# Kernel tuning notes

Measured on AMD Instinct MI355X. Metric: run time of the kernel, lower is better.

The kernel has to match this reference:

```python
import jax, jax.numpy as jnp
import numpy as np

NU, NI, E = 100000, 20000, 250000
H, HEADS, D, L = 128, 2, 64, 2


def setup_inputs() -> dict:
    key = jax.random.key(0)
    ks = jax.random.split(key, 12)
    s = 0.05  # glorot-ish init scale
    return {
        "x_user": jax.random.normal(ks[0], (NU, 64), jnp.float32),
        "x_item": jax.random.normal(ks[1], (NI, 128), jnp.float32),
        "Wp_user": jax.random.normal(ks[2], (64, H), jnp.float32) * s,
        "bp_user": jnp.zeros((H,), jnp.float32),
        "Wp_item": jax.random.normal(ks[3], (128, H), jnp.float32) * s,
        "bp_item": jnp.zeros((H,), jnp.float32),
        # stacked per [layer, relation] params; rel 0 = user->item, rel 1 = item->user
        "Wl": jax.random.normal(ks[4], (L, 2, H, H), jnp.float32) * s,  # source linear
        "bl": jnp.zeros((L, 2, H), jnp.float32),
        "Wr": jax.random.normal(ks[5], (L, 2, H, H), jnp.float32) * s,  # target linear
        "br": jnp.zeros((L, 2, H), jnp.float32),
        "att": jax.random.normal(ks[6], (L, 2, HEADS, D), jnp.float32) * s,
        "bias": jnp.zeros((L, 2, H), jnp.float32),
        "edge_src": jax.random.randint(ks[7], (E,), 0, NU, jnp.int32),  # user index per edge
        "edge_dst": jax.random.randint(ks[8], (E,), 0, NI, jnp.int32),  # item index per edge
    }


def _gatv2(x_src, x_dst, src, dst, wl, bl_, wr, br_, a, b_, n_dst):
    """One bipartite GATv2Conv (heads=HEADS, out=D, concat=True, eval mode)."""
    xl = (x_src @ wl + bl_).reshape(-1, HEADS, D)  # [Ns, h, d]
    xr = (x_dst @ wr + br_).reshape(-1, HEADS, D)  # [Nd, h, d]
    e = jax.nn.leaky_relu(xl[src] + xr[dst], 0.2)  # [E, h, d]
    logits = jnp.einsum('ehd,hd->eh', e, a)        # [E, h]
    # segment softmax over destination nodes (numerically stable)
    amax = jax.lax.stop_gradient(jax.ops.segment_max(logits, dst, num_segments=n_dst))
    p = jnp.exp(logits - amax[dst])
    denom = jax.ops.segment_sum(p, dst, num_segments=n_dst)
    alpha = p / (denom[dst] + 1e-16)               # PyG softmax epsilon
    msg = xl[src] * alpha[:, :, None]              # [E, h, d]
    out = jax.ops.segment_sum(msg, dst, num_segments=n_dst)  # [Nd, h, d]
    return out.reshape(n_dst, HEADS * D) + b_


def reference(x_user, x_item, Wp_user, bp_user, Wp_item, bp_item,
              Wl, bl, Wr, br, att, bias, edge_src, edge_dst):
    zu = x_user @ Wp_user + bp_user  # [NU, H]
    zi = x_item @ Wp_item + bp_item  # [NI, H]
    for l in range(L):
        zi_new = _gatv2(zu, zi, edge_src, edge_dst,
                        Wl[l, 0], bl[l, 0], Wr[l, 0], br[l, 0], att[l, 0], bias[l, 0], NI)
        zu_new = _gatv2(zi, zu, edge_dst, edge_src,
                        Wl[l, 1], bl[l, 1], Wr[l, 1], br[l, 1], att[l, 1], bias[l, 1], NU)
        zu, zi = zu_new, zi_new
        if l < L - 1:
            zu, zi = jax.nn.relu(zu), jax.nn.relu(zi)  # dropout is identity in eval
    return zu, zi
```

## Files before the change

### kernel.cpp

```cpp
#include <hip/hip_runtime.h>

#define HDIM 128

typedef __attribute__((ext_vector_type(8))) short short8;
typedef __attribute__((ext_vector_type(4))) float float4v;

__device__ __forceinline__ float b2f(unsigned short u){
  return __uint_as_float(((unsigned int)u) << 16);
}
__device__ __forceinline__ unsigned short f2b(float f){
  unsigned int x = __float_as_uint(f);
  x += 0x7fffu + ((x >> 16) & 1u);
  return (unsigned short)(x >> 16);
}

#if __has_builtin(__builtin_amdgcn_exp2f)
#define EXPX(x) __builtin_amdgcn_exp2f(x)
#define LOGSCALE 1.4426950408889634f
#else
#define EXPX(x) __expf(x)
#define LOGSCALE 1.f
#endif

__device__ __forceinline__ float dpp_red8(float x){
  x += __int_as_float(__builtin_amdgcn_update_dpp(0, __float_as_int(x), 0xB1, 0xF, 0xF, true));
  x += __int_as_float(__builtin_amdgcn_update_dpp(0, __float_as_int(x), 0x4E, 0xF, 0xF, true));
  x += __int_as_float(__builtin_amdgcn_update_dpp(0, __float_as_int(x), 0x141, 0xF, 0xF, true));
  return x;
}

__device__ __forceinline__ int sniff_block(const unsigned short* __restrict__ x){
  const int tid = threadIdx.x;
  int cnt = 0, tot = 0;
  for (int i = tid * 2; i < 4096; i += 512){
    float v = fabsf(b2f(x[i]));
    tot++;
    if (v > 1e-4f && v < 50.f) cnt++;
  }
  __shared__ int s_cnt[256], s_tot[256];
  s_cnt[tid] = cnt; s_tot[tid] = tot;
  __syncthreads();
  for (int o = 128; o > 0; o >>= 1){
    if (tid < o){ s_cnt[tid] += s_cnt[tid + o]; s_tot[tid] += s_tot[tid + o]; }
    __syncthreads();
  }
  __shared__ int res;
  if (tid == 0) res = (s_cnt[0] * 2 < s_tot[0]) ? 1 : 0;
  __syncthreads();
  return res;
}

#define P_WPU 0
#define P_WPI 8192
#define P_WL  24576
#define P_WR  90112
#define P_BL  155648
#define P_BR  156160
#define P_ATT 156672
#define P_BIA 157184
#define P_BPU 157696
#define P_BPI 157824
#define P_TOT 157952

struct CvtArgs { const void* src[10]; int len[10]; const unsigned short* xsniff; };

__global__ void cvt_all_kernel(CvtArgs args, unsigned short* __restrict__ P,
                               int* __restrict__ flag,
                               int* __restrict__ zero1, int nz1,
                               int* __restrict__ zero2, int nz2){
  const int f32 = sniff_block(args.xsniff);
  int t = blockIdx.x * 256 + threadIdx.x;
  if (t < nz1) zero1[t] = 0;
  if (t < nz2) zero2[t] = 0;
  if (t == 0) flag[0] = f32;
  if (t >= P_TOT) return;
  int local = t;
  int i = 0;
  while (local >= args.len[i]){ local -= args.len[i]; i++; }
  if (f32) P[t] = f2b(((const float*)args.src[i])[local]);
  else     P[t] = ((const unsigned short*)args.src[i])[local];
}

__global__ void prep_count_kernel(const unsigned short* __restrict__ P,
                                  unsigned short* __restrict__ Wc,
                                  const int* __restrict__ esrc, const int* __restrict__ edst,
                                  int* __restrict__ degU, int* __restrict__ degI,
                                  int E, int gPrep)
{
  const int b = blockIdx.x;
  if (b >= gPrep){
    int t = (b - gPrep) * 256 + threadIdx.x;
    if (t < E){
      atomicAdd(&degI[edst[t]], 1);
      atomicAdd(&degU[esrc[t]], 1);
    }
    return;
  }
  const int t = b * 256 + threadIdx.x;
  if (t >= 49664) return;
  const unsigned short* Wl = P + P_WL;
  const unsigned short* Wr = P + P_WR;
  const unsigned short* Bm[4] = { Wl, Wr + 16384, Wl + 16384, Wr };
  const unsigned short* Av[4] = { P + P_WPU, P + P_WPU, P + P_WPI, P + P_WPI };
  const unsigned short* bv[4] = { P + P_BPU, P + P_BPU, P + P_BPI, P + P_BPI };
  const unsigned short* bo[4] = { P + P_BL, P + P_BR + 128, P + P_BL + 128, P + P_BR };
  if (t < 49152){
    int job, base;
    if (t < 8192)       { job = 0; base = 0; }
    else if (t < 16384) { job = 1; base = 8192; }
    else if (t < 32768) { job = 2; base = 16384; }
    else                { job = 3; base = 32768; }
    const int local = t - base;
    const int k = local >> 7, n = local & 127;
    const unsigned short* A = Av[job] + (size_t)k * 128;
    const unsigned short* B = Bm[job];
    float s = 0.f;
    #pragma unroll 4
    for (int h = 0; h < 128; h++) s = fmaf(b2f(A[h]), b2f(B[h * 128 + n]), s);
    Wc[t] = f2b(s);
  } else {
    const int local = t - 49152;
    const int job = local >> 7, n = local & 127;
    const unsigned short* B = Bm[job];
    float s = b2f(bo[job][n]);
    for (int h = 0; h < 128; h++) s = fmaf(b2f(bv[job][h]), b2f(B[h * 128 + n]), s);
    Wc[t] = f2b(s);
  }
}

struct PermBiasArgs { const unsigned short* W0[4]; const unsigned short* W1[4];
                      int KS[4]; int base[4]; int n[4];
                      const unsigned short* blo[4]; const unsigned short* bhi[4]; };

__global__ void permute_scanhist_kernel(PermBiasArgs pa, unsigned short* __restrict__ dst,
                                        unsigned short* __restrict__ dstB, int gPerm,
                                        const int* __restrict__ degI, const int* __restrict__ degU,
                                        int* __restrict__ rpI, int* __restrict__ rpU,
                                        int* __restrict__ blkI, int* __restrict__ blkU,
                                        int* __restrict__ histI, int* __restrict__ histU,
                                        int NI, int NU, int BI, int BU, int BI2, int BU2)
{
  const int tid = threadIdx.x;
  const int bk0 = blockIdx.x;
  if (bk0 < gPerm){
    int t = bk0 * 256 + tid;
    if (t >= 114688){
      int u = t - 114688;
      if (u < 1024){
        int set = u >> 8, c = u & 255;
        dstB[u] = (c < 128) ? pa.blo[set][c] : pa.bhi[set][c - 128];
      }
      return;
    }
    int job = 0;
    while (job < 4 && t >= pa.base[job] + pa.n[job]) job++;
    if (job >= 4) return;
    int local = t - pa.base[job];
    int KS = pa.KS[job];
    int j = local & 7, rest = local >> 3;
    int l = rest & 63; rest >>= 6;
    int ks = rest % KS, tile = rest / KS;
    int k = ks * 32 + (l >> 4) * 8 + j;
    int c = tile * 16 + (l & 15);
    dst[t] = (c < 128) ? pa.W0[job][k * 128 + c] : pa.W1[job][k * 128 + (c - 128)];
    return;
  }
  const int b = bk0 - gPerm;
  const int nscan = BI + BU;
  if (b < nscan){
    __shared__ int s[256];
    const int* deg; int* rowptr; int* blksum; int Nd; int bb;
    if (b < BI){ deg = degI; rowptr = rpI; blksum = blkI; Nd = NI; bb = b; }
    else       { deg = degU; rowptr = rpU; blksum = blkU; Nd = NU; bb = b - BI; }
    const int base = bb * 2048 + tid * 8;
    int v[8]; int tot = 0;
    #pragma unroll
    for (int j = 0; j < 8; j++){
      int idx = base + j;
      v[j] = (idx < Nd) ? deg[idx] : 0;
      tot += v[j];
    }
    s[tid] = tot;
    __syncthreads();
    for (int off = 1; off < 256; off <<= 1){
      int add = (tid >= off) ? s[tid - off] : 0;
      __syncthreads();
      s[tid] += add;
      __syncthreads();
    }
    int run = s[tid] - tot;
    #pragma unroll
    for (int j = 0; j < 8; j++){
      int idx = base + j;
      if (idx < Nd) rowptr[idx] = run;
      run += v[j];
    }
    if (tid == 255) blksum[bb] = s[255];
  } else {
    __shared__ int h2[64];
    if (tid < 64) h2[tid] = 0;
    __syncthreads();
    const int bb = b - nscan;
    const int* deg; int* gh; int base; int N;
    if (bb < BI2){ deg = degI; gh = histI; base = bb * 256; N = NI; }
    else         { deg = degU; gh = histU; base = (bb - BI2) * 256; N = NU; }
    const int n = base + tid;
    if (n < N) atomicAdd(&h2[min(deg[n], 63)], 1);
    __syncthreads();
    if (tid < 64 && h2[tid]) atomicAdd(&gh[tid], h2[tid]);
  }
}

__global__ void scan_add2_kernel(int* __restrict__ rpI, int* __restrict__ rpU,
                                 const int* __restrict__ blkI, const int* __restrict__ blkU,
                                 int* __restrict__ curI, int* __restrict__ curU,
                                 int NI, int NU, int BI, int BU, int E){
  const int b = blockIdx.x;
  int* rowptr; const int* blksum; int* curs; int Nd; int bb; int Bn;
  if (b < BI){ rowptr = rpI; blksum = blkI; curs = curI; Nd = NI; bb = b; Bn = BI; }
  else       { rowptr = rpU; blksum = blkU; curs = curU; Nd = NU; bb = b - BI; Bn = BU; }
  const int tid = threadIdx.x;
  __shared__ int sAdd;
  if (tid < 64){
    int v = (tid < Bn) ? blksum[tid] : 0;
    int x = v;
    #pragma unroll
    for (int off = 1; off < 64; off <<= 1){
      int u = __shfl_up(x, off, 64);
      if (tid >= off) x += u;
    }
    if (tid == bb) sAdd = x - v;
  }
  __syncthreads();
  const int add = sAdd;
  const int base = bb * 2048 + tid * 8;
  #pragma unroll
  for (int j = 0; j < 8; j++){
    int idx = base + j;
    if (idx < Nd){ int v = rowptr[idx] + add; rowptr[idx] = v; curs[idx] = v; }
    else if (idx == Nd) rowptr[idx] = E;
  }
}

__global__ void scatter_all_kernel(const int* __restrict__ esrc, const int* __restrict__ edst,
                                   int* __restrict__ curI, int* __restrict__ curU,
                                   int* __restrict__ srcI, int* __restrict__ srcU,
                                   const int* __restrict__ rpI, const int* __restrict__ rpU,
                                   const int* __restrict__ histI, const int* __restrict__ histU,
                                   int* __restrict__ hcurI, int* __restrict__ hcurU,
                                   int* __restrict__ permI, int* __restrict__ permU,
                                   int NI, int NU, int E, int BI2, int BU2){
  const int tid = threadIdx.x;
  const int b = blockIdx.x;
  const int BP = BI2 + BU2;
  if (b < BP){
    __shared__ int h[64];
    __shared__ int cur[64];
    if (tid < 64) h[tid] = 0;
    __syncthreads();
    const int* rp; const int* gh; int* ghc; int* perm; int base; int N;
    if (b < BI2){ rp = rpI; gh = histI; ghc = hcurI; perm = permI; base = b * 256; N = NI; }
    else        { rp = rpU; gh = histU; ghc = hcurU; perm = permU; base = (b - BI2) * 256; N = NU; }
    const int n = base + tid;
    int bk = -1;
    if (n < N){ int d = rp[n + 1] - rp[n]; bk = min(d, 63); atomicAdd(&h[bk], 1); }
    __syncthreads();
    if (tid < 64){
      int v = gh[tid];
      int x = v;
      #pragma unroll
      for (int off = 1; off < 64; off <<= 1){
        int u = __shfl_down(x, off, 64);
        x += (tid + off < 64) ? u : 0;
      }
      const int suf = x - v;
      cur[tid] = h[tid] ? (suf + atomicAdd(&ghc[tid], h[tid])) : 0;
    }
    __syncthreads();
    if (n < N){ int r = atomicAdd(&cur[bk], 1); perm[r] = n; }
  } else {
    int t = (b - BP) * 256 + tid;
    if (t < E){
      int d = edst[t];
      int pos = atomicAdd(&curI[d], 1);
      srcI[pos] = esrc[t];
    } else if (t < 2 * E){
      int tt = t - E;
      int d = esrc[tt];
      int pos = atomicAdd(&curU[d], 1);
      srcU[pos] = edst[tt];
    }
  }
}

template<int K>
__device__ __forceinline__ void linear_body(const void* __restrict__ Xv, int xstride,
                                            bool f32,
                                            const unsigned short* __restrict__ Bp,
                                            const unsigned short* __restrict__ bias,
                                            unsigned short* __restrict__ Y, int M, int bx,
                                            unsigned short* __restrict__ lds)
{
  constexpr int KS = K / 32;
  constexpr int LK = K + 8;
  constexpr int ROUNDS = (32 * K) / 2048;
  const int wave = threadIdx.x >> 6, lane = threadIdx.x & 63;
  const int quad = lane >> 4, l16 = lane & 15;
  const int row0 = bx * 32;

  #pragma unroll
  for (int rd = 0; rd < ROUNDS; rd++){
    const int e = rd * 2048 + (int)threadIdx.x * 8;
    const int rr = e / K, cc = e % K;
    int grow = row0 + rr; if (grow >= M) grow = M - 1;
    unsigned short* dst = lds + rr * LK + cc;
    if (f32){
      const float* p = (const float*)Xv + (size_t)grow * xstride + cc;
      float4 v0 = *(const float4*)p;
      float4 v1 = *(const float4*)(p + 4);
      short8 tmp;
      tmp[0] = (short)f2b(v0.x); tmp[1] = (short)f2b(v0.y);
      tmp[2] = (short)f2b(v0.z); tmp[3] = (short)f2b(v0.w);
      tmp[4] = (short)f2b(v1.x); tmp[5] = (short)f2b(v1.y);
      tmp[6] = (short)f2b(v1.z); tmp[7] = (short)f2b(v1.w);
      *(short8*)dst = tmp;
    } else {
      *(short8*)dst = *(const short8*)((const unsigned short*)Xv + (size_t)grow * xstride + cc);
    }
  }
  __syncthreads();

  float4v acc[2][4];
  const float4v z = {0.f, 0.f, 0.f, 0.f};
  #pragma unroll
  for (int i = 0; i < 2; i++)
    #pragma unroll
    for (int j = 0; j < 4; j++) acc[i][j] = z;

  #pragma unroll
  for (int ks = 0; ks < KS; ks++){
    const int col = ks * 32 + quad * 8;
    short8 a[2];
    #pragma unroll
    for (int mt = 0; mt < 2; mt++)
      a[mt] = *(const short8*)(lds + (mt * 16 + l16) * LK + col);
    short8 b[4];
    #pragma unroll
    for (int ntl = 0; ntl < 4; ntl++){
      const int t = wave * 4 + ntl;
      b[ntl] = *(const short8*)(Bp + ((size_t)(t * KS + ks) * 64 + lane) * 8);
    }
    #pragma unroll
    for (int mt = 0; mt < 2; mt++)
      #pragma unroll
      for (int ntl = 0; ntl < 4; ntl++)
        acc[mt][ntl] = __builtin_amdgcn_mfma_f32_16x16x32_bf16(a[mt], b[ntl], acc[mt][ntl], 0, 0, 0);
  }

  #pragma unroll
  for (int mt = 0; mt < 2; mt++){
    #pragma unroll
    for (int ntl = 0; ntl < 4; ntl++){
      const int t = wave * 4 + ntl;
      const int colb = t * 16 + l16;
      const float bb = b2f(bias[colb]);
      #pragma unroll
      for (int r = 0; r < 4; r++){
        const int row = row0 + mt * 16 + quad * 4 + r;
        if (row < M) Y[(size_t)row * 256 + colb] = f2b(acc[mt][ntl][r] + bb);
      }
    }
  }
}

template<int KA, int KB>
__launch_bounds__(256)
__global__ void linear_both_kernel(const void* __restrict__ XA, int sA,
                                   const unsigned short* __restrict__ BpA,
                                   const unsigned short* __restrict__ biasA,
                                   unsigned short* __restrict__ YA, int MA, int gA,
                                   const void* __restrict__ XB, int sB,
                                   const unsigned short* __restrict__ BpB,
                                   const unsigned short* __restrict__ biasB,
                                   unsigned short* __restrict__ YB, int MB,
                                   const int* __restrict__ flag, int use_flag)
{
  __shared__ unsigned short lds[32 * 136];
  const bool f32 = use_flag && (*flag != 0);
  if ((int)blockIdx.x < gA) linear_body<KA>(XA, sA, f32, BpA, biasA, YA, MA, blockIdx.x, lds);
  else                      linear_body<KB>(XB, sB, f32, BpB, biasB, YB, MB, blockIdx.x - gA, lds);
}

struct GatRel {
  const unsigned short* zlrS;
  const unsigned short* zlrD;
  const int* rowptr;
  const int* srcArr;
  const int* perm;
  const unsigned short* att;
  const unsigned short* bias;
  void* out;
  unsigned long long elem_off;
  int Nd;
  int nw;
};

__launch_bounds__(256)
__global__ void fused_gat_sorted_kernel(GatRel A, GatRel B, int do_relu,
                                        const int* __restrict__ flag, int final_store)
{
  const int wave = threadIdx.x >> 6;
  const int lane = threadIdx.x & 63;
  const int ql = lane & 15;
  const int quad = lane >> 4;
  int gw = blockIdx.x * 4 + wave;
  GatRel R;
  if (gw < A.nw) R = A;
  else {
    gw -= A.nw;
    if (gw >= B.nw) return;
    R = B;
  }

  const int rank = gw * 4 + quad;
  const bool vnode = rank < R.Nd;
  int d = 0;
  if (vnode) d = R.perm[rank];
  int beg = 0, end = 0;
  if (vnode){ beg = R.rowptr[d]; end = R.rowptr[d + 1]; }
  int md = end - beg;
  md = max(md, __shfl_xor(md, 16, 64));
  md = max(md, __shfl_xor(md, 32, 64));

  const uint4* zlS4 = (const uint4*)R.zlrS;
  uint4 rv = ((const uint4*)R.zlrD)[(size_t)d * 32 + 16 + ql];
  float r[8], a[8];
  {
    const unsigned int* rp = (const unsigned int*)&rv;
    #pragma unroll
    for (int j = 0; j < 4; j++){
      r[2*j]   = __uint_as_float(rp[j] << 16);
      r[2*j+1] = __uint_as_float(rp[j] & 0xffff0000u);
    }
  }
  uint4 av = ((const uint4*)R.att)[ql];
  {
    const unsigned int* ap = (const unsigned int*)&av;
    #pragma unroll
    for (int j = 0; j < 4; j++){
      a[2*j]   = __uint_as_float(ap[j] << 16) * LOGSCALE;
      a[2*j+1] = __uint_as_float(ap[j] & 0xffff0000u) * LOGSCALE;
    }
  }

  float m = -1e30f, s = 0.f;
  float acc[8];
  #pragma unroll
  for (int j = 0; j < 8; j++) acc[j] = 0.f;

  if (md > 0){
    const int* sA = R.srcArr;
    int i1 = 0, i2 = 0;
    if (beg < end)     i1 = sA[beg];
    if (beg + 1 < end) i2 = sA[beg + 1];
    uint4 g0 = zlS4[(size_t)i1 * 32 + ql];

    for (int it = 0; it < md; it++){
      uint4 g1 = zlS4[(size_t)i2 * 32 + ql];
      int i3 = 0;
      { int ee = beg + it + 2; if (ee < end) i3 = sA[ee]; }
      const bool valid = (beg + it) < end;

      float x[8];
      const unsigned int* gp = (const unsigned int*)&g0;
      #pragma unroll
      for (int j = 0; j < 4; j++){
        x[2*j]   = __uint_as_float(gp[j] << 16);
        x[2*j+1] = __uint_as_float(gp[j] & 0xffff0000u);
      }
      float p = 0.f;
      #pragma unroll
      for (int j = 0; j < 8; j++){
        float t = x[j] + r[j];
        t = fmaxf(t, 0.2f * t);
        p = fmaf(a[j], t, p);
      }
      p = dpp_red8(p);
      const float pv = valid ? p : -1e30f;

      if (__builtin_expect(__any(pv > m + 8.f), 0)){
        const float mn = fmaxf(m, pv);
        const float scO = EXPX(m - mn);
        const float qv = valid ? EXPX(pv - mn) : 0.f;
        s = fmaf(s, scO, qv);
        #pragma unroll
        for (int j = 0; j < 8; j++) acc[j] = fmaf(acc[j], scO, x[j] * qv);
        m = mn;
      } else {
        const float qv = valid ? EXPX(pv - m) : 0.f;
        s += qv;
        #pragma unroll
        for (int j = 0; j < 8; j++) acc[j] = fmaf(x[j], qv, acc[j]);
      }
      g0 = g1; i2 = i3;
    }
  }

  const float inv = 1.f / (s + 1e-16f);
  uint4 bv = ((const uint4*)R.bias)[ql];
  float o[8];
  {
    const unsigned int* bp = (const unsigned int*)&bv;
    #pragma unroll
    for (int j = 0; j < 4; j++){
      o[2*j]   = fmaf(acc[2*j],   inv, __uint_as_float(bp[j] << 16));
      o[2*j+1] = fmaf(acc[2*j+1], inv, __uint_as_float(bp[j] & 0xffff0000u));
    }
  }
  if (do_relu){
    #pragma unroll
    for (int j = 0; j < 8; j++) o[j] = fmaxf(o[j], 0.f);
  }
  if (!vnode) return;
  const size_t eidx = (size_t)R.elem_off + (size_t)d * HDIM + 8 * ql;
  if (final_store && (*flag != 0)){
    float4 f0 = {o[0], o[1], o[2], o[3]};
    float4 f1 = {o[4], o[5], o[6], o[7]};
    float4* op = (float4*)R.out;
    op[eidx >> 2] = f0;
    op[(eidx >> 2) + 1] = f1;
  } else {
    uint4 w;
    unsigned int* wp = (unsigned int*)&w;
    #pragma unroll
    for (int j = 0; j < 4; j++)
      wp[j] = (unsigned int)f2b(o[2*j]) | ((unsigned int)f2b(o[2*j+1]) << 16);
    ((uint4*)R.out)[eidx >> 3] = w;
  }
}

extern "C" void kernel_launch(void* const* d_in, const int* in_sizes, int n_in,
                              void* d_out, int out_size, void* d_ws, size_t ws_size,
                              hipStream_t stream)
{
  const int* esrc = (const int*)d_in[12];
  const int* edst = (const int*)d_in[13];

  const int NU = in_sizes[0] / 64;
  const int NI = in_sizes[1] / 128;
  const int E  = in_sizes[12];
  const size_t fu = (size_t)NU * HDIM, fi = (size_t)NI * HDIM;

  char* w = (char*)d_ws;
  auto carve = [&](size_t bytes){ char* p = w; w += (bytes + 255) & ~(size_t)255; return p; };
  int* flag = (int*)carve(4);
  unsigned short* Wc = (unsigned short*)carve(49664 * 2);
  unsigned short* P  = (unsigned short*)carve((size_t)P_TOT * 2);
  unsigned short* Bp = (unsigned short*)carve(114688 * 2);
  unsigned short* Bc = (unsigned short*)carve(1024 * 2);
  int* rowptrI = (int*)carve(((size_t)NI + 1) * 4);
  int* rowptrU = (int*)carve(((size_t)NU + 1) * 4);
  int* curs    = (int*)carve(((size_t)NI + NU) * 4);
  int* cursI = curs;
  int* cursU = curs + NI;
  int* blkI = (int*)carve(64 * 4);
  int* blkU = (int*)carve(64 * 4);
  int* hists = (int*)carve(256 * 4);
  int* histI = hists;
  int* histU = hists + 64;
  int* hcurI = hists + 128;
  int* hcurU = hists + 192;
  int* permI = (int*)carve((size_t)NI * 4);
  int* permU = (int*)carve((size_t)NU * 4);
  int* srcI  = (int*)carve((size_t)E * 4);
  int* srcU  = (int*)carve((size_t)E * 4);
  unsigned short* zlrU = (unsigned short*)carve((size_t)NU * 256 * 2);
  unsigned short* zlrI = (unsigned short*)carve((size_t)NI * 256 * 2);
  (void)ws_size; (void)n_in; (void)out_size; (void)fi;

  unsigned short* stage_zu = (unsigned short*)d_out;
  unsigned short* stage_zi = (unsigned short*)d_out + fu;
  (void)stage_zi;

  CvtArgs ca;
  const int srcIdx[10] = {2, 4, 6, 8, 7, 9, 10, 11, 3, 5};
  const int lens[10] = {8192, 16384, 65536, 65536, 512, 512, 512, 512, 128, 128};
  for (int i = 0; i < 10; i++){ ca.src[i] = d_in[srcIdx[i]]; ca.len[i] = lens[i]; }
  ca.xsniff = (const unsigned short*)d_in[0];
  cvt_all_kernel<<<(P_TOT + 255) / 256, 256, 0, stream>>>(ca, P, flag,
                                                          curs, NI + NU, hists, 256);

  const int gPrep = (49664 + 255) / 256;
  const int gCount = (E + 255) / 256;
  prep_count_kernel<<<gPrep + gCount, 256, 0, stream>>>(P, Wc, esrc, edst,
                                                        cursU, cursI, E, gPrep);

  const unsigned short* cWlU0 = Wc;
  const unsigned short* cWrU1 = Wc + 8192;
  const unsigned short* cWlI1 = Wc + 16384;
  const unsigned short* cWrI0 = Wc + 32768;

  PermBiasArgs pa;
  pa.W0[0] = cWlU0;                 pa.W1[0] = cWrU1;                 pa.KS[0] = 2; pa.base[0] = 0;     pa.n[0] = 16384;
  pa.W0[1] = cWlI1;                 pa.W1[1] = cWrI0;                 pa.KS[1] = 4; pa.base[1] = 16384; pa.n[1] = 32768;
  pa.W0[2] = P + P_WL + 2 * 16384;  pa.W1[2] = P + P_WR + 3 * 16384;  pa.KS[2] = 4; pa.base[2] = 49152; pa.n[2] = 32768;
  pa.W0[3] = P + P_WL + 3 * 16384;  pa.W1[3] = P + P_WR + 2 * 16384;  pa.KS[3] = 4; pa.base[3] = 81920; pa.n[3] = 32768;
  pa.blo[0] = Wc + 49152;         pa.bhi[0] = Wc + 49152 + 128;
  pa.blo[1] = Wc + 49152 + 256;   pa.bhi[1] = Wc + 49152 + 384;
  pa.blo[2] = P + P_BL + 256;     pa.bhi[2] = P + P_BR + 384;
  pa.blo[3] = P + P_BL + 384;     pa.bhi[3] = P + P_BR + 256;
  const int BI = (NI + 2047) / 2048, BU = (NU + 2047) / 2048;
  const int BI2 = (NI + 255) / 256, BU2 = (NU + 255) / 256;
  const int gPerm = (114688 + 1024 + 255) / 256;
  permute_scanhist_kernel<<<gPerm + BI + BU + BI2 + BU2, 256, 0, stream>>>(
      pa, Bp, Bc, gPerm,
      cursI, cursU, rowptrI, rowptrU, blkI, blkU, histI, histU,
      NI, NU, BI, BU, BI2, BU2);
  unsigned short* BpU0 = Bp;
  unsigned short* BpI0 = Bp + 16384;
  unsigned short* BpU1 = Bp + 49152;
  unsigned short* BpI1 = Bp + 81920;

  scan_add2_kernel<<<BI + BU, 256, 0, stream>>>(rowptrI, rowptrU, blkI, blkU,
                                                cursI, cursU, NI, NU, BI, BU, E);
  scatter_all_kernel<<<BI2 + BU2 + (2 * E + 255) / 256, 256, 0, stream>>>(
      esrc, edst, cursI, cursU, srcI, srcU, rowptrI, rowptrU,
      histI, histU, hcurI, hcurU, permI, permU, NI, NU, E, BI2, BU2);

  const int gMU = (NU + 31) / 32, gMI = (NI + 31) / 32;
  const int nwA = (NI + 3) / 4, nwB = (NU + 3) / 4;
  const int gGat = (nwA + nwB + 3) / 4;

  for (int l = 0; l < 2; l++){
    if (l == 0){
      linear_both_kernel<64, 128><<<gMU + gMI, 256, 0, stream>>>(
          d_in[0], 64, BpU0, Bc, zlrU, NU, gMU,
          d_in[1], 128, BpI0, Bc + 256, zlrI, NI, flag, 1);
    } else {
      linear_both_kernel<128, 128><<<gMU + gMI, 256, 0, stream>>>(
          stage_zu, 128, BpU1, Bc + 512, zlrU, NU, gMU,
          stage_zi, 128, BpI1, Bc + 768, zlrI, NI, flag, 0);
    }
    const int relu = (l == 0);
    const int final_store = (l == 1);

    GatRel A, B;
    A.zlrS = zlrU; A.zlrD = zlrI; A.rowptr = rowptrI; A.srcArr = srcI; A.perm = permI;
    A.att  = P + P_ATT + (l * 2 + 0) * HDIM;
    A.bias = P + P_BIA + (l * 2 + 0) * HDIM;
    A.out = final_store ? d_out : (void*)stage_zu; A.elem_off = fu; A.Nd = NI; A.nw = nwA;
    B.zlrS = zlrI; B.zlrD = zlrU; B.rowptr = rowptrU; B.srcArr = srcU; B.perm = permU;
    B.att  = P + P_ATT + (l * 2 + 1) * HDIM;
    B.bias = P + P_BIA + (l * 2 + 1) * HDIM;
    B.out = final_store ? d_out : (void*)stage_zu; B.elem_off = 0; B.Nd = NU; B.nw = nwB;

    fused_gat_sorted_kernel<<<gGat, 256, 0, stream>>>(A, B, relu, flag, final_store);
  }
}
```

Measured before the change: 292.5 us.

## Fuse layer-0 linear into scatter kernel and split counting from weight prep

Layer-0 projection GEMM blocks now run in the same launch as the CSR scatter and perm-building blocks, so independent work overlaps and one launch is dropped. Weight pre-combination now reads raw inputs directly (fp32 or bf16) instead of the converted buffer P. That lets it share a launch with the conversion, while degree counting moves to its own kernel. The kernel count stays roughly the same, but dependencies shift so more independent work is co-scheduled. The trade-off is mixed block types within one grid, and LDS is sized for the larger linear path.

```diff
diff --git a/kernel.cpp b/kernel.cpp
--- a/kernel.cpp
+++ b/kernel.cpp
@@ -12,6 +12,9 @@
   unsigned int x = __float_as_uint(f);
   x += 0x7fffu + ((x >> 16) & 1u);
   return (unsigned short)(x >> 16);
+}
+__device__ __forceinline__ float ldf(const void* p, int idx, bool f32){
+  return f32 ? ((const float*)p)[idx] : b2f(((const unsigned short*)p)[idx]);
 }
 
 #if __has_builtin(__builtin_amdgcn_exp2f)
@@ -63,47 +66,38 @@
 #define P_TOT 157952
 
 struct CvtArgs { const void* src[10]; int len[10]; const unsigned short* xsniff; };
-
-__global__ void cvt_all_kernel(CvtArgs args, unsigned short* __restrict__ P,
-                               int* __restrict__ flag,
-                               int* __restrict__ zero1, int nz1,
-                               int* __restrict__ zero2, int nz2){
-  const int f32 = sniff_block(args.xsniff);
-  int t = blockIdx.x * 256 + threadIdx.x;
-  if (t < nz1) zero1[t] = 0;
-  if (t < nz2) zero2[t] = 0;
-  if (t == 0) flag[0] = f32;
-  if (t >= P_TOT) return;
-  int local = t;
-  int i = 0;
-  while (local >= args.len[i]){ local -= args.len[i]; i++; }
-  if (f32) P[t] = f2b(((const float*)args.src[i])[local]);
-  else     P[t] = ((const unsigned short*)args.src[i])[local];
-}
-
-__global__ void prep_count_kernel(const unsigned short* __restrict__ P,
-                                  unsigned short* __restrict__ Wc,
-                                  const int* __restrict__ esrc, const int* __restrict__ edst,
-                                  int* __restrict__ degU, int* __restrict__ degI,
-                                  int E, int gPrep)
-{
+struct RawW { const void* wpu; const void* bpu; const void* wpi; const void* bpi;
+              const void* wl; const void* bl; const void* wr; const void* br; };
+
+__global__ void cvt_prep_kernel(CvtArgs args, RawW rw,
+                                unsigned short* __restrict__ P,
+                                unsigned short* __restrict__ Wc,
+                                int* __restrict__ flag,
+                                int* __restrict__ zero1, int nz1,
+                                int* __restrict__ zero2, int nz2, int gCvt){
+  const int f32 = sniff_block(args.xsniff) != 0;
   const int b = blockIdx.x;
-  if (b >= gPrep){
-    int t = (b - gPrep) * 256 + threadIdx.x;
-    if (t < E){
-      atomicAdd(&degI[edst[t]], 1);
-      atomicAdd(&degU[esrc[t]], 1);
-    }
+  if (b < gCvt){
+    int t = b * 256 + threadIdx.x;
+    if (t < nz1) zero1[t] = 0;
+    if (t < nz2) zero2[t] = 0;
+    if (t == 0) flag[0] = f32;
+    if (t >= P_TOT) return;
+    int local = t;
+    int i = 0;
+    while (local >= args.len[i]){ local -= args.len[i]; i++; }
+    if (f32) P[t] = f2b(((const float*)args.src[i])[local]);
+    else     P[t] = ((const unsigned short*)args.src[i])[local];
     return;
   }
-  const int t = b * 256 + threadIdx.x;
+  const int t = (b - gCvt) * 256 + threadIdx.x;
   if (t >= 49664) return;
-  const unsigned short* Wl = P + P_WL;
-  const unsigned short* Wr = P + P_WR;
-  const unsigned short* Bm[4] = { Wl, Wr + 16384, Wl + 16384, Wr };
-  const unsigned short* Av[4] = { P + P_WPU, P + P_WPU, P + P_WPI, P + P_WPI };
-  const unsigned short* bv[4] = { P + P_BPU, P + P_BPU, P + P_BPI, P + P_BPI };
-  const unsigned short* bo[4] = { P + P_BL, P + P_BR + 128, P + P_BL + 128, P + P_BR };
+  const void* Bm[4] = { rw.wl, rw.wr, rw.wl, rw.wr };
+  const int  BmO[4] = { 0, 16384, 16384, 0 };
+  const void* Av[4] = { rw.wpu, rw.wpu, rw.wpi, rw.wpi };
+  const void* bv[4] = { rw.bpu, rw.bpu, rw.bpi, rw.bpi };
+  const void* bo[4] = { rw.bl, rw.br, rw.bl, rw.br };
+  const int  boO[4] = { 0, 128, 128, 0 };
   if (t < 49152){
     int job, base;
     if (t < 8192)       { job = 0; base = 0; }
@@ -112,20 +106,27 @@
     else                { job = 3; base = 32768; }
     const int local = t - base;
     const int k = local >> 7, n = local & 127;
-    const unsigned short* A = Av[job] + (size_t)k * 128;
-    const unsigned short* B = Bm[job];
     float s = 0.f;
     #pragma unroll 4
-    for (int h = 0; h < 128; h++) s = fmaf(b2f(A[h]), b2f(B[h * 128 + n]), s);
+    for (int h = 0; h < 128; h++)
+      s = fmaf(ldf(Av[job], k * 128 + h, f32), ldf(Bm[job], BmO[job] + h * 128 + n, f32), s);
     Wc[t] = f2b(s);
   } else {
     const int local = t - 49152;
     const int job = local >> 7, n = local & 127;
-    const unsigned short* B = Bm[job];
-    float s = b2f(bo[job][n]);
-    for (int h = 0; h < 128; h++) s = fmaf(b2f(bv[job][h]), b2f(B[h * 128 + n]), s);
+    float s = ldf(bo[job], boO[job] + n, f32);
+    for (int h = 0; h < 128; h++)
+      s = fmaf(ldf(bv[job], h, f32), ldf(Bm[job], BmO[job] + h * 128 + n, f32), s);
     Wc[t] = f2b(s);
   }
+}
+
+__global__ void count_kernel(const int* __restrict__ esrc, const int* __restrict__ edst,
+                             int* __restrict__ degU, int* __restrict__ degI, int E){
+  int t = blockIdx.x * 256 + threadIdx.x;
+  if (t >= E) return;
+  atomicAdd(&degI[edst[t]], 1);
+  atomicAdd(&degU[esrc[t]], 1);
 }
 
 struct PermBiasArgs { const unsigned short* W0[4]; const unsigned short* W1[4];
@@ -242,20 +243,118 @@
   }
 }
 
-__global__ void scatter_all_kernel(const int* __restrict__ esrc, const int* __restrict__ edst,
-                                   int* __restrict__ curI, int* __restrict__ curU,
-                                   int* __restrict__ srcI, int* __restrict__ srcU,
-                                   const int* __restrict__ rpI, const int* __restrict__ rpU,
-                                   const int* __restrict__ histI, const int* __restrict__ histU,
-                                   int* __restrict__ hcurI, int* __restrict__ hcurU,
-                                   int* __restrict__ permI, int* __restrict__ permU,
-                                   int NI, int NU, int E, int BI2, int BU2){
+template<int K>
+__device__ __forceinline__ void linear_body(const void* __restrict__ Xv, int xstride,
+                                            bool f32,
+                                            const unsigned short* __restrict__ Bp,
+                                            const unsigned short* __restrict__ bias,
+                                            unsigned short* __restrict__ Y, int M, int bx,
+                                            unsigned short* __restrict__ lds)
+{
+  constexpr int KS = K / 32;
+  constexpr int LK = K + 8;
+  constexpr int ROUNDS = (32 * K) / 2048;
+  const int wave = threadIdx.x >> 6, lane = threadIdx.x & 63;
+  const int quad = lane >> 4, l16 = lane & 15;
+  const int row0 = bx * 32;
+
+  #pragma unroll
+  for (int rd = 0; rd < ROUNDS; rd++){
+    const int e = rd * 2048 + (int)threadIdx.x * 8;
+    const int rr = e / K, cc = e % K;
+    int grow = row0 + rr; if (grow >= M) grow = M - 1;
+    unsigned short* dst = lds + rr * LK + cc;
+    if (f32){
+      const float* p = (const float*)Xv + (size_t)grow * xstride + cc;
+      float4 v0 = *(const float4*)p;
+      float4 v1 = *(const float4*)(p + 4);
+      short8 tmp;
+      tmp[0] = (short)f2b(v0.x); tmp[1] = (short)f2b(v0.y);
+      tmp[2] = (short)f2b(v0.z); tmp[3] = (short)f2b(v0.w);
+      tmp[4] = (short)f2b(v1.x); tmp[5] = (short)f2b(v1.y);
+      tmp[6] = (short)f2b(v1.z); tmp[7] = (short)f2b(v1.w);
+      *(short8*)dst = tmp;
+    } else {
+      *(short8*)dst = *(const short8*)((const unsigned short*)Xv + (size_t)grow * xstride + cc);
+    }
+  }
+  __syncthreads();
+
+  float4v acc[2][4];
+  const float4v z = {0.f, 0.f, 0.f, 0.f};
+  #pragma unroll
+  for (int i = 0; i < 2; i++)
+    #pragma unroll
+    for (int j = 0; j < 4; j++) acc[i][j] = z;
+
+  #pragma unroll
+  for (int ks = 0; ks < KS; ks++){
+    const int col = ks * 32 + quad * 8;
+    short8 a[2];
+    #pragma unroll
+    for (int mt = 0; mt < 2; mt++)
+      a[mt] = *(const short8*)(lds + (mt * 16 + l16) * LK + col);
+    short8 b[4];
+    #pragma unroll
+    for (int ntl = 0; ntl < 4; ntl++){
+      const int t = wave * 4 + ntl;
+      b[ntl] = *(const short8*)(Bp + ((size_t)(t * KS + ks) * 64 + lane) * 8);
+    }
+    #pragma unroll
+    for (int mt = 0; mt < 2; mt++)
+      #pragma unroll
+      for (int ntl = 0; ntl < 4; ntl++)
+        acc[mt][ntl] = __builtin_amdgcn_mfma_f32_16x16x32_bf16(a[mt], b[ntl], acc[mt][ntl], 0, 0, 0);
+  }
+
+  #pragma unroll
+  for (int mt = 0; mt < 2; mt++){
+    #pragma unroll
+    for (int ntl = 0; ntl < 4; ntl++){
+      const int t = wave * 4 + ntl;
+      const int colb = t * 16 + l16;
+      const float bb = b2f(bias[colb]);
+      #pragma unroll
+      for (int r = 0; r < 4; r++){
+        const int row = row0 + mt * 16 + quad * 4 + r;
+        if (row < M) Y[(size_t)row * 256 + colb] = f2b(acc[mt][ntl][r] + bb);
+      }
+    }
+  }
+}
+
+template<int KA, int KB>
+__launch_bounds__(256)
+__global__ void scatter_lin_kernel(
+    const void* __restrict__ XA, int sA, const unsigned short* __restrict__ BpA,
+    const unsigned short* __restrict__ biasA, unsigned short* __restrict__ YA, int MA, int gA,
+    const void* __restrict__ XB, int sB, const unsigned short* __restrict__ BpB,
+    const unsigned short* __restrict__ biasB, unsigned short* __restrict__ YB, int MB, int gB,
+    const int* __restrict__ flag, int use_flag,
+    const int* __restrict__ esrc, const int* __restrict__ edst,
+    int* __restrict__ curI, int* __restrict__ curU,
+    int* __restrict__ srcI, int* __restrict__ srcU,
+    const int* __restrict__ rpI, const int* __restrict__ rpU,
+    const int* __restrict__ histI, const int* __restrict__ histU,
+    int* __restrict__ hcurI, int* __restrict__ hcurU,
+    int* __restrict__ permI, int* __restrict__ permU,
+    int NI, int NU, int E, int BI2, int BU2)
+{
+  __shared__ unsigned short lds[32 * 136];
   const int tid = threadIdx.x;
-  const int b = blockIdx.x;
+  const int gLin = gA + gB;
+  const int b0 = blockIdx.x;
+  if (b0 < gLin){
+    const bool f32 = use_flag && (*flag != 0);
+    if (b0 < gA) linear_body<KA>(XA, sA, f32, BpA, biasA, YA, MA, b0, lds);
+    else         linear_body<KB>(XB, sB, f32, BpB, biasB, YB, MB, b0 - gA, lds);
+    return;
+  }
+  const int b = b0 - gLin;
   const int BP = BI2 + BU2;
   if (b < BP){
-    __shared__ int h[64];
-    __shared__ int cur[64];
+    int* h = (int*)lds;
+    int* cur = (int*)lds + 64;
     if (tid < 64) h[tid] = 0;
     __syncthreads();
     const int* rp; const int* gh; int* ghc; int* perm; int base; int N;
@@ -289,86 +388,6 @@
       int d = esrc[tt];
       int pos = atomicAdd(&curU[d], 1);
       srcU[pos] = edst[tt];
-    }
-  }
-}
-
-template<int K>
-__device__ __forceinline__ void linear_body(const void* __restrict__ Xv, int xstride,
-                                            bool f32,
-                                            const unsigned short* __restrict__ Bp,
-                                            const unsigned short* __restrict__ bias,
-                                            unsigned short* __restrict__ Y, int M, int bx,
-                                            unsigned short* __restrict__ lds)
-{
-  constexpr int KS = K / 32;
-  constexpr int LK = K + 8;
-  constexpr int ROUNDS = (32 * K) / 2048;
-  const int wave = threadIdx.x >> 6, lane = threadIdx.x & 63;
-  const int quad = lane >> 4, l16 = lane & 15;
-  const int row0 = bx * 32;
-
-  #pragma unroll
-  for (int rd = 0; rd < ROUNDS; rd++){
-    const int e = rd * 2048 + (int)threadIdx.x * 8;
-    const int rr = e / K, cc = e % K;
-    int grow = row0 + rr; if (grow >= M) grow = M - 1;
-    unsigned short* dst = lds + rr * LK + cc;
-    if (f32){
-      const float* p = (const float*)Xv + (size_t)grow * xstride + cc;
-      float4 v0 = *(const float4*)p;
-      float4 v1 = *(const float4*)(p + 4);
-      short8 tmp;
-      tmp[0] = (short)f2b(v0.x); tmp[1] = (short)f2b(v0.y);
-      tmp[2] = (short)f2b(v0.z); tmp[3] = (short)f2b(v0.w);
-      tmp[4] = (short)f2b(v1.x); tmp[5] = (short)f2b(v1.y);
-      tmp[6] = (short)f2b(v1.z); tmp[7] = (short)f2b(v1.w);
-      *(short8*)dst = tmp;
-    } else {
-      *(short8*)dst = *(const short8*)((const unsigned short*)Xv + (size_t)grow * xstride + cc);
-    }
-  }
-  __syncthreads();
-
-  float4v acc[2][4];
-  const float4v z = {0.f, 0.f, 0.f, 0.f};
-  #pragma unroll
-  for (int i = 0; i < 2; i++)
-    #pragma unroll
-    for (int j = 0; j < 4; j++) acc[i][j] = z;
-
-  #pragma unroll
-  for (int ks = 0; ks < KS; ks++){
-    const int col = ks * 32 + quad * 8;
-    short8 a[2];
-    #pragma unroll
-    for (int mt = 0; mt < 2; mt++)
-      a[mt] = *(const short8*)(lds + (mt * 16 + l16) * LK + col);
-    short8 b[4];
-    #pragma unroll
-    for (int ntl = 0; ntl < 4; ntl++){
-      const int t = wave * 4 + ntl;
-      b[ntl] = *(const short8*)(Bp + ((size_t)(t * KS + ks) * 64 + lane) * 8);
-    }
-    #pragma unroll
-    for (int mt = 0; mt < 2; mt++)
-      #pragma unroll
-      for (int ntl = 0; ntl < 4; ntl++)
-        acc[mt][ntl] = __builtin_amdgcn_mfma_f32_16x16x32_bf16(a[mt], b[ntl], acc[mt][ntl], 0, 0, 0);
-  }
-
-  #pragma unroll
-  for (int mt = 0; mt < 2; mt++){
-    #pragma unroll
-    for (int ntl = 0; ntl < 4; ntl++){
-      const int t = wave * 4 + ntl;
-      const int colb = t * 16 + l16;
-      const float bb = b2f(bias[colb]);
-      #pragma unroll
-      for (int r = 0; r < 4; r++){
-        const int row = row0 + mt * 16 + quad * 4 + r;
-        if (row < M) Y[(size_t)row * 256 + colb] = f2b(acc[mt][ntl][r] + bb);
-      }
     }
   }
 }
@@ -587,13 +606,15 @@
   const int lens[10] = {8192, 16384, 65536, 65536, 512, 512, 512, 512, 128, 128};
   for (int i = 0; i < 10; i++){ ca.src[i] = d_in[srcIdx[i]]; ca.len[i] = lens[i]; }
   ca.xsniff = (const unsigned short*)d_in[0];
-  cvt_all_kernel<<<(P_TOT + 255) / 256, 256, 0, stream>>>(ca, P, flag,
-                                                          curs, NI + NU, hists, 256);
-
+  RawW rw;
+  rw.wpu = d_in[2]; rw.bpu = d_in[3]; rw.wpi = d_in[4]; rw.bpi = d_in[5];
+  rw.wl  = d_in[6]; rw.bl  = d_in[7]; rw.wr  = d_in[8]; rw.br  = d_in[9];
+  const int gCvt = (P_TOT + 255) / 256;
   const int gPrep = (49664 + 255) / 256;
-  const int gCount = (E + 255) / 256;
-  prep_count_kernel<<<gPrep + gCount, 256, 0, stream>>>(P, Wc, esrc, edst,
-                                                        cursU, cursI, E, gPrep);
+  cvt_prep_kernel<<<gCvt + gPrep, 256, 0, stream>>>(ca, rw, P, Wc, flag,
+                                                    curs, NI + NU, hists, 256, gCvt);
+
+  count_kernel<<<(E + 255) / 256, 256, 0, stream>>>(esrc, edst, cursU, cursI, E);
 
   const unsigned short* cWlU0 = Wc;
   const unsigned short* cWrU1 = Wc + 8192;
@@ -623,20 +644,22 @@
 
   scan_add2_kernel<<<BI + BU, 256, 0, stream>>>(rowptrI, rowptrU, blkI, blkU,
                                                 cursI, cursU, NI, NU, BI, BU, E);
-  scatter_all_kernel<<<BI2 + BU2 + (2 * E + 255) / 256, 256, 0, stream>>>(
+
+  const int gMU = (NU + 31) / 32, gMI = (NI + 31) / 32;
+  const int gE = (2 * E + 255) / 256;
+
+  scatter_lin_kernel<64, 128><<<gMU + gMI + BI2 + BU2 + gE, 256, 0, stream>>>(
+      d_in[0], 64, BpU0, Bc, zlrU, NU, gMU,
+      d_in[1], 128, BpI0, Bc + 256, zlrI, NI, gMI,
+      flag, 1,
       esrc, edst, cursI, cursU, srcI, srcU, rowptrI, rowptrU,
       histI, histU, hcurI, hcurU, permI, permU, NI, NU, E, BI2, BU2);
 
-  const int gMU = (NU + 31) / 32, gMI = (NI + 31) / 32;
   const int nwA = (NI + 3) / 4, nwB = (NU + 3) / 4;
   const int gGat = (nwA + nwB + 3) / 4;
 
   for (int l = 0; l < 2; l++){
-    if (l == 0){
-      linear_both_kernel<64, 128><<<gMU + gMI, 256, 0, stream>>>(
-          d_in[0], 64, BpU0, Bc, zlrU, NU, gMU,
-          d_in[1], 128, BpI0, Bc + 256, zlrI, NI, flag, 1);
-    } else {
+    if (l == 1){
       linear_both_kernel<128, 128><<<gMU + gMI, 256, 0, stream>>>(
           stage_zu, 128, BpU1, Bc + 512, zlrU, NU, gMU,
           stage_zi, 128, BpI1, Bc + 768, zlrI, NI, flag, 0);
```

Measured after the change: 308.2 us. 1.05x slower.
